# Performance work log

Measured on AMD Instinct MI355X. Metric: run time of the kernel, lower is better.

Reference implementation:

```python
import jax, jax.numpy as jnp
import numpy as np

N_NODES = 50000
N_EDGES = 400000
DIM = 64
HEADS = 8
NUM_GRAPHS = 64
OUT_DIM = 32
NEG_SLOPE = 0.2
EPS = 1e-5


def setup_inputs() -> dict:
    key = jax.random.key(0)
    ks = jax.random.split(key, 20)
    inp = {
        "x": jax.random.normal(ks[0], (N_NODES, DIM), dtype=jnp.float32),
        "edge_index": jax.random.randint(ks[1], (2, N_EDGES), 0, N_NODES, dtype=jnp.int64),
        "batch": jnp.sort(jax.random.randint(ks[2], (N_NODES,), 0, NUM_GRAPHS, dtype=jnp.int64)),
    }
    s = 0.05
    # GATConv layer 1 (in=DIM, out=DIM per head, heads=HEADS, concat=False)
    inp["W1"] = jax.random.normal(ks[3], (DIM, HEADS * DIM), dtype=jnp.float32) * s
    inp["a_src1"] = jax.random.normal(ks[4], (HEADS, DIM), dtype=jnp.float32) * s
    inp["a_dst1"] = jax.random.normal(ks[5], (HEADS, DIM), dtype=jnp.float32) * s
    inp["b1"] = jnp.zeros((DIM,), dtype=jnp.float32)
    inp["ln1_w"] = jnp.ones((DIM,), dtype=jnp.float32)
    inp["ln1_b"] = jnp.zeros((DIM,), dtype=jnp.float32)
    # GATConv layer 2
    inp["W2"] = jax.random.normal(ks[6], (DIM, HEADS * DIM), dtype=jnp.float32) * s
    inp["a_src2"] = jax.random.normal(ks[7], (HEADS, DIM), dtype=jnp.float32) * s
    inp["a_dst2"] = jax.random.normal(ks[8], (HEADS, DIM), dtype=jnp.float32) * s
    inp["b2"] = jnp.zeros((DIM,), dtype=jnp.float32)
    inp["ln2_w"] = jnp.ones((DIM,), dtype=jnp.float32)
    inp["ln2_b"] = jnp.zeros((DIM,), dtype=jnp.float32)
    # DownStream head
    inp["Wh"] = jax.random.normal(ks[9], (DIM, OUT_DIM), dtype=jnp.float32) * s
    inp["bh"] = jnp.zeros((OUT_DIM,), dtype=jnp.float32)
    return inp


def _edge_softmax(logits, dst, n):
    # per-destination-node softmax over incoming edges; logits: [E, H]
    m = jax.ops.segment_max(logits, dst, num_segments=n)
    e = jnp.exp(logits - m[dst])
    s = jax.ops.segment_sum(e, dst, num_segments=n)
    return e / (s[dst] + 1e-16)


def _gat_conv(x, src, dst, W, a_src, a_dst, b):
    # PyG GATConv, heads=HEADS, concat=False (mean over heads), eval mode (no dropout)
    n = x.shape[0]
    h = (x @ W).reshape(n, HEADS, -1)              # [N, H, D]
    al_s = jnp.einsum("nhd,hd->nh", h, a_src)      # [N, H]
    al_d = jnp.einsum("nhd,hd->nh", h, a_dst)
    logits = jax.nn.leaky_relu(al_s[src] + al_d[dst], NEG_SLOPE)  # [E, H]
    alpha = _edge_softmax(logits, dst, n)
    out = jax.ops.segment_sum(alpha[:, :, None] * h[src], dst, num_segments=n)  # [N, H, D]
    return out.mean(axis=1) + b


def _graph_layer_norm(x, batch, w, b):
    # PyG LayerNorm mode='graph': normalize over all nodes and channels of each graph
    f = x.shape[1]
    cnt = jax.ops.segment_sum(jnp.ones((x.shape[0],), x.dtype), batch, num_segments=NUM_GRAPHS)
    norm = jnp.clip(cnt, 1.0) * f
    mean = jax.ops.segment_sum(x.sum(axis=-1), batch, num_segments=NUM_GRAPHS) / norm
    xc = x - mean[batch][:, None]
    var = jax.ops.segment_sum((xc * xc).sum(axis=-1), batch, num_segments=NUM_GRAPHS) / norm
    out = xc * jax.lax.rsqrt(var + EPS)[batch][:, None]
    return out * w + b


def reference(x, edge_index, batch, W1, a_src1, a_dst1, b1, ln1_w, ln1_b,
              W2, a_src2, a_dst2, b2, ln2_w, ln2_b, Wh, bh):
    n = x.shape[0]
    loops = jnp.arange(n, dtype=edge_index.dtype)
    src = jnp.concatenate([edge_index[0], loops])   # add_self_loops (PyG default)
    dst = jnp.concatenate([edge_index[1], loops])

    # My_GATConv (dropout is identity in eval)
    h = x + _gat_conv(x, src, dst, W1, a_src1, a_dst1, b1)
    h = jax.nn.relu(_graph_layer_norm(h, batch, ln1_w, ln1_b))
    h = h + _gat_conv(h, src, dst, W2, a_src2, a_dst2, b2)
    h = jax.nn.relu(_graph_layer_norm(h, batch, ln2_w, ln2_b))

    # global_mean_pool over batch
    cnt = jax.ops.segment_sum(jnp.ones((n,), h.dtype), batch, num_segments=NUM_GRAPHS)
    pooled = jax.ops.segment_sum(h, batch, num_segments=NUM_GRAPHS) / jnp.clip(cnt, 1.0)[:, None]

    # DownStream head
    return jax.nn.relu(pooled @ Wh + bh)
```

## Files before the change

### kernel.cpp

```cpp
#include <hip/hip_runtime.h>
#include <math.h>

#define N_NODES 50000
#define N_EDGES 400000
#define E_TOT   (N_EDGES + N_NODES)
#define NG      64
#define NEG_SLOPE 0.2f

typedef __attribute__((ext_vector_type(8))) short bf16x8;
typedef __attribute__((ext_vector_type(4))) float f32x4;

__device__ __forceinline__ float wave_sum(float v){
#pragma unroll
  for (int off = 32; off; off >>= 1) v += __shfl_xor(v, off, 64);
  return v;
}
__device__ __forceinline__ float lrelu(float x){ return x > 0.f ? x : NEG_SLOPE * x; }
__device__ __forceinline__ ushort f2bf(float f){
  union { float f; unsigned u; } v; v.f = f;
  unsigned r = v.u + 0x7FFFu + ((v.u >> 16) & 1u);
  return (ushort)(r >> 16);
}
__device__ __forceinline__ float bf2f(ushort u){
  return __uint_as_float(((unsigned)u) << 16);
}
__device__ __forceinline__ float bflo(unsigned u){ return __uint_as_float(u << 16); }
__device__ __forceinline__ float bfhi(unsigned u){ return __uint_as_float(u & 0xffff0000u); }

__device__ __forceinline__ void acc8(float* acc, uint4 w, float xv){
  acc[0] = fmaf(bflo(w.x), xv, acc[0]);
  acc[1] = fmaf(bfhi(w.x), xv, acc[1]);
  acc[2] = fmaf(bflo(w.y), xv, acc[2]);
  acc[3] = fmaf(bfhi(w.y), xv, acc[3]);
  acc[4] = fmaf(bflo(w.z), xv, acc[4]);
  acc[5] = fmaf(bfhi(w.z), xv, acc[5]);
  acc[6] = fmaf(bflo(w.w), xv, acc[6]);
  acc[7] = fmaf(bfhi(w.w), xv, acc[7]);
}

__global__ void prep_all_kernel(const float* __restrict__ W1, const float* __restrict__ as1,
                                const float* __restrict__ ad1, const float* __restrict__ W2,
                                const float* __restrict__ as2, const float* __restrict__ ad2,
                                float* __restrict__ wa1, float* __restrict__ wa2,
                                ushort* __restrict__ w1pT, ushort* __restrict__ w2pT){
  int idx = blockIdx.x * blockDim.x + threadIdx.x;
  if (idx < 2048){
    const float* W = (idx < 1024) ? W1 : W2;
    const float* asr = (idx < 1024) ? as1 : as2;
    const float* adr = (idx < 1024) ? ad1 : ad2;
    float* wa = (idx < 1024) ? wa1 : wa2;
    int i = idx & 1023;
    int k = i >> 4, c = i & 15;
    int h = c & 7;
    const float* a = (c < 8) ? asr : adr;
    float s = 0.f;
#pragma unroll
    for (int d = 0; d < 64; ++d) s = fmaf(W[k * 512 + h * 64 + d], a[h * 64 + d], s);
    wa[i] = s;
  } else if (idx < 2048 + 2 * 32768){
    int i = idx - 2048;
    const float* W = (i < 32768) ? W1 : W2;
    ushort* wpT = (i < 32768) ? w1pT : w2pT;
    i &= 32767;
    int j = i >> 9, k = i & 511;
    int h = k >> 6, d = k & 63;
    wpT[i] = f2bf(W[d * 512 + h * 64 + j] * 0.125f);
  }
}

__global__ void graph_bounds_kernel(const int* __restrict__ batch, int* __restrict__ gstart){
  int n = blockIdx.x * blockDim.x + threadIdx.x;
  if (n > N_NODES) return;
  int g = (n < N_NODES) ? batch[n] : NG;
  if (n == 0){
    for (int gg = 0; gg <= g; ++gg) gstart[gg] = 0;
  } else {
    int gp = batch[n - 1];
    for (int gg = gp + 1; gg <= g; ++gg) gstart[gg] = n;
  }
}

__global__ void count_kernel(const int* __restrict__ ei, int* __restrict__ counts){
  int e = blockIdx.x * blockDim.x + threadIdx.x;
  if (e >= E_TOT) return;
  int dst = (e < N_EDGES) ? ei[N_EDGES + e] : (e - N_EDGES);
  atomicAdd(&counts[dst], 1);
}

#define SCAN_B 1024
#define SCAN_NB ((N_NODES + SCAN_B - 1) / SCAN_B)

__global__ __launch_bounds__(SCAN_B) void scan1_kernel(const int* __restrict__ counts,
                                                       int* __restrict__ row_off,
                                                       int* __restrict__ blocksum){
  __shared__ int sh[SCAN_B];
  int i = blockIdx.x * SCAN_B + threadIdx.x;
  int v = (i < N_NODES) ? counts[i] : 0;
  sh[threadIdx.x] = v;
  __syncthreads();
#pragma unroll
  for (int off = 1; off < SCAN_B; off <<= 1){
    int add = (threadIdx.x >= (unsigned)off) ? sh[threadIdx.x - off] : 0;
    __syncthreads();
    sh[threadIdx.x] += add;
    __syncthreads();
  }
  if (i < N_NODES) row_off[i] = sh[threadIdx.x] - v;
  if (threadIdx.x == SCAN_B - 1) blocksum[blockIdx.x] = sh[SCAN_B - 1];
}

__global__ void scan2_kernel(int* __restrict__ blocksum, int* __restrict__ blockoff){
  __shared__ int sh[64];
  int t = threadIdx.x;
  int v = (t < SCAN_NB) ? blocksum[t] : 0;
  sh[t] = v;
  __syncthreads();
#pragma unroll
  for (int off = 1; off < 64; off <<= 1){
    int add = (t >= off) ? sh[t - off] : 0;
    __syncthreads();
    sh[t] += add;
    __syncthreads();
  }
  if (t < SCAN_NB) blockoff[t] = sh[t] - v;
  if (t == 63) blockoff[SCAN_NB] = sh[63];
}

__global__ void scan3_kernel(int* __restrict__ row_off, const int* __restrict__ blockoff){
  int i = blockIdx.x * blockDim.x + threadIdx.x;
  if (i < N_NODES) row_off[i] += blockoff[i >> 10];
  if (i == 0) row_off[N_NODES] = blockoff[SCAN_NB];
}

__global__ void scatter_kernel(const int* __restrict__ ei, const int* __restrict__ row_off,
                               int* __restrict__ cursor, int* __restrict__ csr_src){
  int e = blockIdx.x * blockDim.x + threadIdx.x;
  if (e >= E_TOT) return;
  int src, dst;
  if (e < N_EDGES){ src = ei[e]; dst = ei[N_EDGES + e]; }
  else            { src = dst = e - N_EDGES; }
  int pos = row_off[dst] + atomicAdd(&cursor[dst], 1);
  csr_src[pos] = src;
}

__global__ void al1_kernel(const float* __restrict__ xin, const float* __restrict__ wa,
                           float* __restrict__ al, ushort* __restrict__ xbf){
  __shared__ float w[64 * 16];
  for (int i = threadIdx.x; i < 1024; i += blockDim.x) w[i] = wa[i];
  __syncthreads();
  int idx = blockIdx.x * blockDim.x + threadIdx.x;
  if (idx >= N_NODES * 16) return;
  int n = idx >> 4, c = idx & 15;
  const float* xr = xin + (size_t)n * 64;
  float s = 0.f;
  ushort ob[4];
#pragma unroll
  for (int k4 = 0; k4 < 16; ++k4){
    float4 v = *(const float4*)(xr + k4 * 4);
    s = fmaf(v.x, w[(k4 * 4 + 0) * 16 + c], s);
    s = fmaf(v.y, w[(k4 * 4 + 1) * 16 + c], s);
    s = fmaf(v.z, w[(k4 * 4 + 2) * 16 + c], s);
    s = fmaf(v.w, w[(k4 * 4 + 3) * 16 + c], s);
    if (k4 == c >> 2){
      int rot = c & 3;
    }
  }
  float4 mine = *(const float4*)(xr + c * 4);
  ob[0] = f2bf(mine.x); ob[1] = f2bf(mine.y); ob[2] = f2bf(mine.z); ob[3] = f2bf(mine.w);
  *(ushort4*)(xbf + (size_t)n * 64 + c * 4) = *(const ushort4*)ob;
  al[idx] = s;
}

__global__ void al2_kernel(const ushort* __restrict__ xin, const float* __restrict__ wa,
                           float* __restrict__ al){
  __shared__ float w[64 * 16];
  for (int i = threadIdx.x; i < 1024; i += blockDim.x) w[i] = wa[i];
  __syncthreads();
  int idx = blockIdx.x * blockDim.x + threadIdx.x;
  if (idx >= N_NODES * 16) return;
  int n = idx >> 4, c = idx & 15;
  const ushort* xr = xin + (size_t)n * 64;
  float s = 0.f;
#pragma unroll
  for (int k8 = 0; k8 < 8; ++k8){
    uint4 u = *(const uint4*)(xr + k8 * 8);
    unsigned uu[4] = {u.x, u.y, u.z, u.w};
#pragma unroll
    for (int j = 0; j < 4; ++j){
      int k = k8 * 8 + j * 2;
      s = fmaf(bflo(uu[j]), w[k * 16 + c], s);
      s = fmaf(bfhi(uu[j]), w[(k + 1) * 16 + c], s);
    }
  }
  al[idx] = s;
}

__global__ void weights_kernel(const float* __restrict__ al, const int* __restrict__ row_off,
                               const int* __restrict__ csr_src, ushort* __restrict__ ewb){
  int wid = (int)((blockIdx.x * blockDim.x + threadIdx.x) >> 6);
  int lane = threadIdx.x & 63;
  if (wid >= N_NODES) return;
  const int n = wid;
  const int eo = lane >> 3, h = lane & 7;
  const int s0 = row_off[n], s1 = row_off[n + 1];
  const float ald = al[n * 16 + 8 + h];

  if (s1 - s0 <= 64){
    float wv[8];
    float sum = 0.f;
#pragma unroll
    for (int i = 0; i < 8; ++i){
      int e = s0 + eo + i * 8;
      float v = 0.f;
      if (e < s1){
        int s = csr_src[e];
        v = __expf(lrelu(al[s * 16 + h] + ald));
      }
      wv[i] = v;
      sum += v;
    }
#pragma unroll
    for (int off = 8; off < 64; off <<= 1) sum += __shfl_xor(sum, off, 64);
    float inv = 1.f / (sum + 1e-16f);
#pragma unroll
    for (int i = 0; i < 8; ++i){
      int e = s0 + eo + i * 8;
      if (e < s1) ewb[(size_t)e * 8 + h] = f2bf(wv[i] * inv);
    }
  } else {
    float sum = 0.f;
    for (int e = s0 + eo; e < s1; e += 8){
      int s = csr_src[e];
      sum += __expf(lrelu(al[s * 16 + h] + ald));
    }
#pragma unroll
    for (int off = 8; off < 64; off <<= 1) sum += __shfl_xor(sum, off, 64);
    float inv = 1.f / (sum + 1e-16f);
    for (int e = s0 + eo; e < s1; e += 8){
      int s = csr_src[e];
      ewb[(size_t)e * 8 + h] = f2bf(__expf(lrelu(al[s * 16 + h] + ald)) * inv);
    }
  }
}

__global__ void agg2_kernel(const ushort* __restrict__ xb, const ushort* __restrict__ ewb,
                            const int* __restrict__ row_off, const int* __restrict__ csr_src,
                            ushort* __restrict__ aggx){
  int wid = (int)((blockIdx.x * blockDim.x + threadIdx.x) >> 6);
  int lane = threadIdx.x & 63;
  if (wid >= N_NODES) return;
  const int n = wid;
  const int s0 = row_off[n], s1 = row_off[n + 1];
  float acc[8];
#pragma unroll
  for (int h = 0; h < 8; ++h) acc[h] = 0.f;

  int e = s0;
  for (; e + 4 <= s1; e += 4){
    int sa = csr_src[e], sb = csr_src[e + 1], sc = csr_src[e + 2], sd = csr_src[e + 3];
    float xa = bf2f(xb[(size_t)sa * 64 + lane]);
    float xc = bf2f(xb[(size_t)sb * 64 + lane]);
    float xe = bf2f(xb[(size_t)sc * 64 + lane]);
    float xg = bf2f(xb[(size_t)sd * 64 + lane]);
    uint4 wa = *(const uint4*)(ewb + (size_t)e * 8);
    uint4 wb = *(const uint4*)(ewb + (size_t)(e + 1) * 8);
    uint4 wc = *(const uint4*)(ewb + (size_t)(e + 2) * 8);
    uint4 wd = *(const uint4*)(ewb + (size_t)(e + 3) * 8);
    acc8(acc, wa, xa);
    acc8(acc, wb, xc);
    acc8(acc, wc, xe);
    acc8(acc, wd, xg);
  }
  for (; e < s1; ++e){
    int sa = csr_src[e];
    float xa = bf2f(xb[(size_t)sa * 64 + lane]);
    uint4 wa = *(const uint4*)(ewb + (size_t)e * 8);
    acc8(acc, wa, xa);
  }
#pragma unroll
  for (int h = 0; h < 8; ++h)
    aggx[(size_t)n * 512 + h * 64 + lane] = f2bf(acc[h]);
}

__global__ __launch_bounds__(256) void outgemm_stats_kernel(const ushort* __restrict__ A,
                                                            const ushort* __restrict__ BT,
                                                            const float* __restrict__ bias,
                                                            const float* __restrict__ res,
                                                            const int* __restrict__ batch,
                                                            float* __restrict__ Y,
                                                            float* __restrict__ gs,
                                                            float* __restrict__ gss){
  __shared__ ushort Al[64][136];
  __shared__ ushort Bl[64][136];
  __shared__ float gsl[NG], gssl[NG];
  const int t = threadIdx.x;
  const int wave = t >> 6, lane = t & 63;
  const int rowbase = blockIdx.x * 64;
  const int frow = lane & 15, kc = lane >> 4;
  if (t < NG){ gsl[t] = 0.f; gssl[t] = 0.f; }
  f32x4 acc[4];
#pragma unroll
  for (int ct = 0; ct < 4; ++ct) acc[ct] = (f32x4){0.f, 0.f, 0.f, 0.f};

  for (int k0 = 0; k0 < 512; k0 += 128){
#pragma unroll
    for (int ppass = 0; ppass < 4; ++ppass){
      int idx = (ppass * 256 + t) * 8;
      int r = idx >> 7, k = idx & 127;
      int grow = rowbase + r;
      uint4 v = make_uint4(0u, 0u, 0u, 0u);
      if (grow < N_NODES) v = *(const uint4*)(A + (size_t)grow * 512 + k0 + k);
      *(uint4*)&Al[r][k] = v;
      uint4 w = *(const uint4*)(BT + (size_t)r * 512 + k0 + k);
      *(uint4*)&Bl[r][k] = w;
    }
    __syncthreads();
#pragma unroll
    for (int kf = 0; kf < 4; ++kf){
      bf16x8 a = *(const bf16x8*)&Al[wave * 16 + frow][kf * 32 + kc * 8];
#pragma unroll
      for (int ct = 0; ct < 4; ++ct){
        bf16x8 b = *(const bf16x8*)&Bl[ct * 16 + frow][kf * 32 + kc * 8];
        acc[ct] = __builtin_amdgcn_mfma_f32_16x16x32_bf16(a, b, acc[ct], 0, 0, 0);
      }
    }
    __syncthreads();
  }
  const int col0 = lane & 15, rsub = (lane >> 4) * 4;
  float rs[4] = {0.f, 0.f, 0.f, 0.f}, rss[4] = {0.f, 0.f, 0.f, 0.f};
#pragma unroll
  for (int ct = 0; ct < 4; ++ct){
    int col = ct * 16 + col0;
    float bs = bias[col];
#pragma unroll
    for (int j = 0; j < 4; ++j){
      int grow = rowbase + wave * 16 + rsub + j;
      if (grow < N_NODES){
        float y = acc[ct][j] + bs + res[(size_t)grow * 64 + col];
        Y[(size_t)grow * 64 + col] = y;
        rs[j] += y;
        rss[j] = fmaf(y, y, rss[j]);
      }
    }
  }
#pragma unroll
  for (int j = 0; j < 4; ++j){
#pragma unroll
    for (int off = 1; off < 16; off <<= 1){
      rs[j] += __shfl_xor(rs[j], off, 64);
      rss[j] += __shfl_xor(rss[j], off, 64);
    }
  }
  if (col0 == 0){
#pragma unroll
    for (int j = 0; j < 4; ++j){
      int grow = rowbase + wave * 16 + rsub + j;
      if (grow < N_NODES){
        int g = batch[grow];
        atomicAdd(&gsl[g], rs[j]);
        atomicAdd(&gssl[g], rss[j]);
      }
    }
  }
  __syncthreads();
  if (t < NG && (gsl[t] != 0.f || gssl[t] != 0.f)){
    atomicAdd(&gs[t], gsl[t]);
    atomicAdd(&gss[t], gssl[t]);
  }
}

__global__ void norm_relu_kernel(const float* __restrict__ Y, const int* __restrict__ batch,
                                 const int* __restrict__ gstart, const float* __restrict__ gs,
                                 const float* __restrict__ gss,
                                 const float* __restrict__ lw, const float* __restrict__ lb,
                                 float* __restrict__ out, ushort* __restrict__ outb){
  int idx = blockIdx.x * blockDim.x + threadIdx.x;
  if (idx >= N_NODES * 64) return;
  int n = idx >> 6, c = idx & 63;
  int g = batch[n];
  float cnt = (float)(gstart[g + 1] - gstart[g]);
  float norm = fmaxf(cnt, 1.f) * 64.f;
  float m = gs[g] / norm;
  float var = fmaxf(gss[g] / norm - m * m, 0.f);
  float rstd = rsqrtf(var + 1e-5f);
  float v = (Y[idx] - m) * rstd * lw[c] + lb[c];
  float r = fmaxf(v, 0.f);
  out[idx] = r;
  outb[idx] = f2bf(r);
}

__global__ void norm_relu_pool_kernel(const float* __restrict__ Y, const int* __restrict__ batch,
                                      const int* __restrict__ gstart, const float* __restrict__ gs,
                                      const float* __restrict__ gss,
                                      const float* __restrict__ lw, const float* __restrict__ lb,
                                      float* __restrict__ pooled){
  int w = (int)((blockIdx.x * blockDim.x + threadIdx.x) >> 6);
  int lane = threadIdx.x & 63;
  int nbase = w * 16;
  if (nbase >= N_NODES) return;
  int nend = min(nbase + 16, N_NODES);
  float accv = 0.f;
  int g = batch[nbase];
  float cnt = (float)(gstart[g + 1] - gstart[g]);
  float norm = fmaxf(cnt, 1.f) * 64.f;
  float m = gs[g] / norm;
  float var = fmaxf(gss[g] / norm - m * m, 0.f);
  float rstd = rsqrtf(var + 1e-5f);
  for (int n = nbase; n < nend; ++n){
    int gn = batch[n];
    if (gn != g){
      atomicAdd(&pooled[g * 64 + lane], accv);
      accv = 0.f; g = gn;
      cnt = (float)(gstart[g + 1] - gstart[g]);
      norm = fmaxf(cnt, 1.f) * 64.f;
      m = gs[g] / norm;
      var = fmaxf(gss[g] / norm - m * m, 0.f);
      rstd = rsqrtf(var + 1e-5f);
    }
    float v = (Y[(size_t)n * 64 + lane] - m) * rstd * lw[lane] + lb[lane];
    accv += fmaxf(v, 0.f);
  }
  atomicAdd(&pooled[g * 64 + lane], accv);
}

__global__ void head_kernel(const float* __restrict__ pooled, const int* __restrict__ gstart,
                            const float* __restrict__ Wh, const float* __restrict__ bh,
                            float* __restrict__ out){
  int idx = blockIdx.x * blockDim.x + threadIdx.x;
  if (idx >= NG * 32) return;
  int g = idx >> 5, o = idx & 31;
  float cnt = (float)(gstart[g + 1] - gstart[g]);
  float inv = 1.f / fmaxf(cnt, 1.f);
  float s = 0.f;
#pragma unroll
  for (int d = 0; d < 64; ++d) s = fmaf(pooled[g * 64 + d] * inv, Wh[d * 32 + o], s);
  out[idx] = fmaxf(s + bh[o], 0.f);
}

extern "C" void kernel_launch(void* const* d_in, const int* in_sizes, int n_in,
                              void* d_out, int out_size, void* d_ws, size_t ws_size,
                              hipStream_t stream){
  const float* x     = (const float*)d_in[0];
  const int*   ei    = (const int*)d_in[1];
  const int*   batch = (const int*)d_in[2];
  const float* W1    = (const float*)d_in[3];
  const float* as1   = (const float*)d_in[4];
  const float* ad1   = (const float*)d_in[5];
  const float* b1    = (const float*)d_in[6];
  const float* l1w   = (const float*)d_in[7];
  const float* l1b   = (const float*)d_in[8];
  const float* W2    = (const float*)d_in[9];
  const float* as2   = (const float*)d_in[10];
  const float* ad2   = (const float*)d_in[11];
  const float* b2    = (const float*)d_in[12];
  const float* l2w   = (const float*)d_in[13];
  const float* l2b   = (const float*)d_in[14];
  const float* Wh    = (const float*)d_in[15];
  const float* bh    = (const float*)d_in[16];
  float* out = (float*)d_out;

  char* p = (char*)d_ws;
  auto alloc = [&](size_t bytes) -> void* {
    void* r = (void*)p;
    p += (bytes + 255) & ~(size_t)255;
    return r;
  };
  int*    counts   = (int*)alloc(N_NODES * 4);
  int*    cursor   = (int*)alloc(N_NODES * 4);
  int*    row_off  = (int*)alloc((N_NODES + 1) * 4);
  int*    csr_src  = (int*)alloc(E_TOT * 4);
  int*    gstart   = (int*)alloc((NG + 1) * 4);
  int*    blocksum = (int*)alloc((SCAN_NB + 1) * 4);
  int*    blockoff = (int*)alloc((SCAN_NB + 1) * 4);
  float*  wa1      = (float*)alloc(64 * 16 * 4);
  float*  wa2      = (float*)alloc(64 * 16 * 4);
  ushort* w1pT     = (ushort*)alloc(64 * 512 * 2);
  ushort* w2pT     = (ushort*)alloc(64 * 512 * 2);
  float*  al       = (float*)alloc((size_t)N_NODES * 16 * 4);
  ushort* ewb      = (ushort*)alloc((size_t)E_TOT * 8 * 2);
  ushort* xbf      = (ushort*)alloc((size_t)N_NODES * 64 * 2);
  ushort* y1b      = (ushort*)alloc((size_t)N_NODES * 64 * 2);
  ushort* aggx     = (ushort*)alloc((size_t)N_NODES * 512 * 2);
  float*  y1p      = (float*)alloc((size_t)N_NODES * 64 * 4);
  float*  y1       = (float*)alloc((size_t)N_NODES * 64 * 4);
  float*  y2p      = y1p;
  float*  gstats   = (float*)alloc(8 * NG * 4);
  float*  pooled   = (float*)alloc(NG * 64 * 4);
  float* gs1 = gstats, *gss1 = gstats + NG, *gs2 = gstats + 2*NG, *gss2 = gstats + 3*NG;

  hipMemsetAsync(counts, 0, (size_t)((char*)row_off - (char*)counts), stream);
  hipMemsetAsync(gstats, 0, (size_t)((char*)pooled - (char*)gstats) + NG * 64 * 4, stream);

  prep_all_kernel<<<(2048 + 2 * 32768 + 255) / 256, 256, 0, stream>>>(
      W1, as1, ad1, W2, as2, ad2, wa1, wa2, w1pT, w2pT);

  graph_bounds_kernel<<<(N_NODES + 256) / 256, 256, 0, stream>>>(batch, gstart);

  count_kernel<<<(E_TOT + 255) / 256, 256, 0, stream>>>(ei, counts);
  scan1_kernel<<<SCAN_NB, SCAN_B, 0, stream>>>(counts, row_off, blocksum);
  scan2_kernel<<<1, 64, 0, stream>>>(blocksum, blockoff);
  scan3_kernel<<<(N_NODES + 255) / 256, 256, 0, stream>>>(row_off, blockoff);
  scatter_kernel<<<(E_TOT + 255) / 256, 256, 0, stream>>>(ei, row_off, cursor, csr_src);

  const int aggBlocks  = (N_NODES + 3) / 4;
  const int waveBlocks = ((N_NODES + 15) / 16 * 64 + 255) / 256;
  const int gemmBlocks = (N_NODES + 63) / 64;

  al1_kernel<<<(N_NODES * 16 + 255) / 256, 256, 0, stream>>>(x, wa1, al, xbf);
  weights_kernel<<<aggBlocks, 256, 0, stream>>>(al, row_off, csr_src, ewb);
  agg2_kernel<<<aggBlocks, 256, 0, stream>>>(xbf, ewb, row_off, csr_src, aggx);
  outgemm_stats_kernel<<<gemmBlocks, 256, 0, stream>>>(aggx, w1pT, b1, x, batch, y1p, gs1, gss1);
  norm_relu_kernel<<<(N_NODES * 64 + 255) / 256, 256, 0, stream>>>(y1p, batch, gstart, gs1, gss1, l1w, l1b, y1, y1b);

  al2_kernel<<<(N_NODES * 16 + 255) / 256, 256, 0, stream>>>(y1b, wa2, al);
  weights_kernel<<<aggBlocks, 256, 0, stream>>>(al, row_off, csr_src, ewb);
  agg2_kernel<<<aggBlocks, 256, 0, stream>>>(y1b, ewb, row_off, csr_src, aggx);
  outgemm_stats_kernel<<<gemmBlocks, 256, 0, stream>>>(aggx, w2pT, b2, y1, batch, y2p, gs2, gss2);
  norm_relu_pool_kernel<<<waveBlocks, 256, 0, stream>>>(y2p, batch, gstart, gs2, gss2, l2w, l2b, pooled);

  head_kernel<<<(NG * 32 + 255) / 256, 256, 0, stream>>>(pooled, gstart, Wh, bh, out);
}
```

Before: 250.0 us.

## Fuse edge-softmax weights into aggregation and merge setup kernels

The separate weights and aggregation kernels are merged into one wagg kernel. It computes per-edge softmax weights, stages them in shared memory per wave, and consumes them immediately, so the global ewb edge-weight buffer is no longer written and re-read. The prep, graph-bounds and count kernels are also merged into a single setup launch to cut launch overhead. In exchange, the block-wide __syncthreads with a chunk count set by the max degree across the four nodes in a block couples the waves, and the slow path recomputes the exp per chunk.

```diff
diff --git a/kernel.cpp b/kernel.cpp
--- a/kernel.cpp
+++ b/kernel.cpp
@@ -10,11 +10,6 @@
 typedef __attribute__((ext_vector_type(8))) short bf16x8;
 typedef __attribute__((ext_vector_type(4))) float f32x4;
 
-__device__ __forceinline__ float wave_sum(float v){
-#pragma unroll
-  for (int off = 32; off; off >>= 1) v += __shfl_xor(v, off, 64);
-  return v;
-}
 __device__ __forceinline__ float lrelu(float x){ return x > 0.f ? x : NEG_SLOPE * x; }
 __device__ __forceinline__ ushort f2bf(float f){
   union { float f; unsigned u; } v; v.f = f;
@@ -38,11 +33,17 @@
   acc[7] = fmaf(bfhi(w.w), xv, acc[7]);
 }
 
-__global__ void prep_all_kernel(const float* __restrict__ W1, const float* __restrict__ as1,
-                                const float* __restrict__ ad1, const float* __restrict__ W2,
-                                const float* __restrict__ as2, const float* __restrict__ ad2,
-                                float* __restrict__ wa1, float* __restrict__ wa2,
-                                ushort* __restrict__ w1pT, ushort* __restrict__ w2pT){
+#define SETUP_PREP   (2048 + 2 * 32768)
+#define SETUP_BOUNDS (SETUP_PREP + N_NODES + 1)
+#define SETUP_TOTAL  (SETUP_BOUNDS + E_TOT)
+
+__global__ void setup_kernel(const float* __restrict__ W1, const float* __restrict__ as1,
+                             const float* __restrict__ ad1, const float* __restrict__ W2,
+                             const float* __restrict__ as2, const float* __restrict__ ad2,
+                             const int* __restrict__ batch, const int* __restrict__ ei,
+                             float* __restrict__ wa1, float* __restrict__ wa2,
+                             ushort* __restrict__ w1pT, ushort* __restrict__ w2pT,
+                             int* __restrict__ gstart, int* __restrict__ counts){
   int idx = blockIdx.x * blockDim.x + threadIdx.x;
   if (idx < 2048){
     const float* W = (idx < 1024) ? W1 : W2;
@@ -57,7 +58,7 @@
 #pragma unroll
     for (int d = 0; d < 64; ++d) s = fmaf(W[k * 512 + h * 64 + d], a[h * 64 + d], s);
     wa[i] = s;
-  } else if (idx < 2048 + 2 * 32768){
+  } else if (idx < SETUP_PREP){
     int i = idx - 2048;
     const float* W = (i < 32768) ? W1 : W2;
     ushort* wpT = (i < 32768) ? w1pT : w2pT;
@@ -65,26 +66,20 @@
     int j = i >> 9, k = i & 511;
     int h = k >> 6, d = k & 63;
     wpT[i] = f2bf(W[d * 512 + h * 64 + j] * 0.125f);
-  }
-}
-
-__global__ void graph_bounds_kernel(const int* __restrict__ batch, int* __restrict__ gstart){
-  int n = blockIdx.x * blockDim.x + threadIdx.x;
-  if (n > N_NODES) return;
-  int g = (n < N_NODES) ? batch[n] : NG;
-  if (n == 0){
-    for (int gg = 0; gg <= g; ++gg) gstart[gg] = 0;
-  } else {
-    int gp = batch[n - 1];
-    for (int gg = gp + 1; gg <= g; ++gg) gstart[gg] = n;
-  }
-}
-
-__global__ void count_kernel(const int* __restrict__ ei, int* __restrict__ counts){
-  int e = blockIdx.x * blockDim.x + threadIdx.x;
-  if (e >= E_TOT) return;
-  int dst = (e < N_EDGES) ? ei[N_EDGES + e] : (e - N_EDGES);
-  atomicAdd(&counts[dst], 1);
+  } else if (idx < SETUP_BOUNDS){
+    int n = idx - SETUP_PREP;
+    int g = (n < N_NODES) ? batch[n] : NG;
+    if (n == 0){
+      for (int gg = 0; gg <= g; ++gg) gstart[gg] = 0;
+    } else {
+      int gp = batch[n - 1];
+      for (int gg = gp + 1; gg <= g; ++gg) gstart[gg] = n;
+    }
+  } else if (idx < SETUP_TOTAL){
+    int e = idx - SETUP_BOUNDS;
+    int dst = (e < N_EDGES) ? ei[N_EDGES + e] : (e - N_EDGES);
+    atomicAdd(&counts[dst], 1);
+  }
 }
 
 #define SCAN_B 1024
@@ -153,7 +148,6 @@
   int n = idx >> 4, c = idx & 15;
   const float* xr = xin + (size_t)n * 64;
   float s = 0.f;
-  ushort ob[4];
 #pragma unroll
   for (int k4 = 0; k4 < 16; ++k4){
     float4 v = *(const float4*)(xr + k4 * 4);
@@ -161,12 +155,9 @@
     s = fmaf(v.y, w[(k4 * 4 + 1) * 16 + c], s);
     s = fmaf(v.z, w[(k4 * 4 + 2) * 16 + c], s);
     s = fmaf(v.w, w[(k4 * 4 + 3) * 16 + c], s);
-    if (k4 == c >> 2){
-      int rot = c & 3;
-    }
   }
   float4 mine = *(const float4*)(xr + c * 4);
-  ob[0] = f2bf(mine.x); ob[1] = f2bf(mine.y); ob[2] = f2bf(mine.z); ob[3] = f2bf(mine.w);
+  ushort ob[4] = {f2bf(mine.x), f2bf(mine.y), f2bf(mine.z), f2bf(mine.w)};
   *(ushort4*)(xbf + (size_t)n * 64 + c * 4) = *(const ushort4*)ob;
   al[idx] = s;
 }
@@ -195,91 +186,99 @@
   al[idx] = s;
 }
 
-__global__ void weights_kernel(const float* __restrict__ al, const int* __restrict__ row_off,
-                               const int* __restrict__ csr_src, ushort* __restrict__ ewb){
-  int wid = (int)((blockIdx.x * blockDim.x + threadIdx.x) >> 6);
-  int lane = threadIdx.x & 63;
-  if (wid >= N_NODES) return;
-  const int n = wid;
+__global__ __launch_bounds__(256) void wagg_kernel(const ushort* __restrict__ xb,
+                                                   const float* __restrict__ al,
+                                                   const int* __restrict__ row_off,
+                                                   const int* __restrict__ csr_src,
+                                                   ushort* __restrict__ aggx){
+  __shared__ ushort ws[4][64][8];
+  __shared__ int sdeg[4];
+  const int wave = threadIdx.x >> 6, lane = threadIdx.x & 63;
+  const int n = blockIdx.x * 4 + wave;
+  const int s0 = row_off[n], s1 = row_off[n + 1];
+  const int deg = s1 - s0;
+  if (lane == 0) sdeg[wave] = deg;
+  __syncthreads();
+  const int mdeg = max(max(sdeg[0], sdeg[1]), max(sdeg[2], sdeg[3]));
+  const int nchunk = (mdeg + 63) >> 6;
+
   const int eo = lane >> 3, h = lane & 7;
-  const int s0 = row_off[n], s1 = row_off[n + 1];
   const float ald = al[n * 16 + 8 + h];
 
-  if (s1 - s0 <= 64){
-    float wv[8];
-    float sum = 0.f;
+  const bool fast = (deg <= 64);
+  float wv[8];
+  float sum = 0.f;
+  if (fast){
 #pragma unroll
     for (int i = 0; i < 8; ++i){
       int e = s0 + eo + i * 8;
       float v = 0.f;
-      if (e < s1){
-        int s = csr_src[e];
-        v = __expf(lrelu(al[s * 16 + h] + ald));
-      }
-      wv[i] = v;
-      sum += v;
-    }
-#pragma unroll
-    for (int off = 8; off < 64; off <<= 1) sum += __shfl_xor(sum, off, 64);
-    float inv = 1.f / (sum + 1e-16f);
-#pragma unroll
-    for (int i = 0; i < 8; ++i){
-      int e = s0 + eo + i * 8;
-      if (e < s1) ewb[(size_t)e * 8 + h] = f2bf(wv[i] * inv);
+      if (e < s1){ int s = csr_src[e]; v = __expf(lrelu(al[s * 16 + h] + ald)); }
+      wv[i] = v; sum += v;
     }
   } else {
-    float sum = 0.f;
     for (int e = s0 + eo; e < s1; e += 8){
       int s = csr_src[e];
       sum += __expf(lrelu(al[s * 16 + h] + ald));
     }
-#pragma unroll
-    for (int off = 8; off < 64; off <<= 1) sum += __shfl_xor(sum, off, 64);
-    float inv = 1.f / (sum + 1e-16f);
-    for (int e = s0 + eo; e < s1; e += 8){
-      int s = csr_src[e];
-      ewb[(size_t)e * 8 + h] = f2bf(__expf(lrelu(al[s * 16 + h] + ald)) * inv);
-    }
-  }
-}
-
-__global__ void agg2_kernel(const ushort* __restrict__ xb, const ushort* __restrict__ ewb,
-                            const int* __restrict__ row_off, const int* __restrict__ csr_src,
-                            ushort* __restrict__ aggx){
-  int wid = (int)((blockIdx.x * blockDim.x + threadIdx.x) >> 6);
-  int lane = threadIdx.x & 63;
-  if (wid >= N_NODES) return;
-  const int n = wid;
-  const int s0 = row_off[n], s1 = row_off[n + 1];
+  }
+#pragma unroll
+  for (int off = 8; off < 64; off <<= 1) sum += __shfl_xor(sum, off, 64);
+  const float inv = 1.f / (sum + 1e-16f);
+
   float acc[8];
 #pragma unroll
-  for (int h = 0; h < 8; ++h) acc[h] = 0.f;
-
-  int e = s0;
-  for (; e + 4 <= s1; e += 4){
-    int sa = csr_src[e], sb = csr_src[e + 1], sc = csr_src[e + 2], sd = csr_src[e + 3];
-    float xa = bf2f(xb[(size_t)sa * 64 + lane]);
-    float xc = bf2f(xb[(size_t)sb * 64 + lane]);
-    float xe = bf2f(xb[(size_t)sc * 64 + lane]);
-    float xg = bf2f(xb[(size_t)sd * 64 + lane]);
-    uint4 wa = *(const uint4*)(ewb + (size_t)e * 8);
-    uint4 wb = *(const uint4*)(ewb + (size_t)(e + 1) * 8);
-    uint4 wc = *(const uint4*)(ewb + (size_t)(e + 2) * 8);
-    uint4 wd = *(const uint4*)(ewb + (size_t)(e + 3) * 8);
-    acc8(acc, wa, xa);
-    acc8(acc, wb, xc);
-    acc8(acc, wc, xe);
-    acc8(acc, wd, xg);
-  }
-  for (; e < s1; ++e){
-    int sa = csr_src[e];
-    float xa = bf2f(xb[(size_t)sa * 64 + lane]);
-    uint4 wa = *(const uint4*)(ewb + (size_t)e * 8);
-    acc8(acc, wa, xa);
-  }
-#pragma unroll
-  for (int h = 0; h < 8; ++h)
-    aggx[(size_t)n * 512 + h * 64 + lane] = f2bf(acc[h]);
+  for (int i = 0; i < 8; ++i) acc[i] = 0.f;
+
+  for (int c = 0; c < nchunk; ++c){
+    const int base = s0 + c * 64;
+    if (fast){
+      if (c == 0){
+#pragma unroll
+        for (int i = 0; i < 8; ++i){
+          int e = s0 + eo + i * 8;
+          if (e < s1) ws[wave][eo + i * 8][h] = f2bf(wv[i] * inv);
+        }
+      }
+    } else {
+#pragma unroll
+      for (int i = 0; i < 8; ++i){
+        int e = base + eo + i * 8;
+        if (e < s1){
+          int s = csr_src[e];
+          ws[wave][e - base][h] = f2bf(__expf(lrelu(al[s * 16 + h] + ald)) * inv);
+        }
+      }
+    }
+    __syncthreads();
+    const int cend = min(base + 64, s1);
+    int e = base;
+    for (; e + 4 <= cend; e += 4){
+      int sa = csr_src[e], sb = csr_src[e + 1], sc = csr_src[e + 2], sd = csr_src[e + 3];
+      float xa = bf2f(xb[(size_t)sa * 64 + lane]);
+      float xc = bf2f(xb[(size_t)sb * 64 + lane]);
+      float xe = bf2f(xb[(size_t)sc * 64 + lane]);
+      float xg = bf2f(xb[(size_t)sd * 64 + lane]);
+      uint4 wa = *(const uint4*)ws[wave][e - base];
+      uint4 wb = *(const uint4*)ws[wave][e - base + 1];
+      uint4 wc = *(const uint4*)ws[wave][e - base + 2];
+      uint4 wd = *(const uint4*)ws[wave][e - base + 3];
+      acc8(acc, wa, xa);
+      acc8(acc, wb, xc);
+      acc8(acc, wc, xe);
+      acc8(acc, wd, xg);
+    }
+    for (; e < cend; ++e){
+      int sa = csr_src[e];
+      float xa = bf2f(xb[(size_t)sa * 64 + lane]);
+      uint4 wa = *(const uint4*)ws[wave][e - base];
+      acc8(acc, wa, xa);
+    }
+    __syncthreads();
+  }
+#pragma unroll
+  for (int i = 0; i < 8; ++i)
+    aggx[(size_t)n * 512 + i * 64 + lane] = f2bf(acc[i]);
 }
 
 __global__ __launch_bounds__(256) void outgemm_stats_kernel(const ushort* __restrict__ A,
@@ -477,7 +476,6 @@
   ushort* w1pT     = (ushort*)alloc(64 * 512 * 2);
   ushort* w2pT     = (ushort*)alloc(64 * 512 * 2);
   float*  al       = (float*)alloc((size_t)N_NODES * 16 * 4);
-  ushort* ewb      = (ushort*)alloc((size_t)E_TOT * 8 * 2);
   ushort* xbf      = (ushort*)alloc((size_t)N_NODES * 64 * 2);
   ushort* y1b      = (ushort*)alloc((size_t)N_NODES * 64 * 2);
   ushort* aggx     = (ushort*)alloc((size_t)N_NODES * 512 * 2);
@@ -491,30 +489,25 @@
   hipMemsetAsync(counts, 0, (size_t)((char*)row_off - (char*)counts), stream);
   hipMemsetAsync(gstats, 0, (size_t)((char*)pooled - (char*)gstats) + NG * 64 * 4, stream);
 
-  prep_all_kernel<<<(2048 + 2 * 32768 + 255) / 256, 256, 0, stream>>>(
-      W1, as1, ad1, W2, as2, ad2, wa1, wa2, w1pT, w2pT);
-
-  graph_bounds_kernel<<<(N_NODES + 256) / 256, 256, 0, stream>>>(batch, gstart);
-
-  count_kernel<<<(E_TOT + 255) / 256, 256, 0, stream>>>(ei, counts);
+  setup_kernel<<<(SETUP_TOTAL + 255) / 256, 256, 0, stream>>>(
+      W1, as1, ad1, W2, as2, ad2, batch, ei, wa1, wa2, w1pT, w2pT, gstart, counts);
+
   scan1_kernel<<<SCAN_NB, SCAN_B, 0, stream>>>(counts, row_off, blocksum);
   scan2_kernel<<<1, 64, 0, stream>>>(blocksum, blockoff);
   scan3_kernel<<<(N_NODES + 255) / 256, 256, 0, stream>>>(row_off, blockoff);
   scatter_kernel<<<(E_TOT + 255) / 256, 256, 0, stream>>>(ei, row_off, cursor, csr_src);
 
-  const int aggBlocks  = (N_NODES + 3) / 4;
+  const int waggBlocks = N_NODES / 4;
   const int waveBlocks = ((N_NODES + 15) / 16 * 64 + 255) / 256;
   const int gemmBlocks = (N_NODES + 63) / 64;
 
   al1_kernel<<<(N_NODES * 16 + 255) / 256, 256, 0, stream>>>(x, wa1, al, xbf);
-  weights_kernel<<<aggBlocks, 256, 0, stream>>>(al, row_off, csr_src, ewb);
-  agg2_kernel<<<aggBlocks, 256, 0, stream>>>(xbf, ewb, row_off, csr_src, aggx);
+  wagg_kernel<<<waggBlocks, 256, 0, stream>>>(xbf, al, row_off, csr_src, aggx);
   outgemm_stats_kernel<<<gemmBlocks, 256, 0, stream>>>(aggx, w1pT, b1, x, batch, y1p, gs1, gss1);
   norm_relu_kernel<<<(N_NODES * 64 + 255) / 256, 256, 0, stream>>>(y1p, batch, gstart, gs1, gss1, l1w, l1b, y1, y1b);
 
   al2_kernel<<<(N_NODES * 16 + 255) / 256, 256, 0, stream>>>(y1b, wa2, al);
-  weights_kernel<<<aggBlocks, 256, 0, stream>>>(al, row_off, csr_src, ewb);
-  agg2_kernel<<<aggBlocks, 256, 0, stream>>>(y1b, ewb, row_off, csr_src, aggx);
+  wagg_kernel<<<waggBlocks, 256, 0, stream>>>(y1b, al, row_off, csr_src, aggx);
   outgemm_stats_kernel<<<gemmBlocks, 256, 0, stream>>>(aggx, w2pT, b2, y1, batch, y2p, gs2, gss2);
   norm_relu_pool_kernel<<<waveBlocks, 256, 0, stream>>>(y2p, batch, gstart, gs2, gss2, l2w, l2b, pooled);
 
```

After: 251.4 us. No clear change (+0.6%).
